# Performance work log

Hardware: AMD Instinct MI355X
Metric: run time of the kernel (lower is better)

The kernel has to match this reference:

```python
import jax, jax.numpy as jnp
import numpy as np

QUERY_DIM = 3072
HEADS = 24
HEAD_DIM = 128
INNER = HEADS * HEAD_DIM  # 3072
MLP_HIDDEN = int(QUERY_DIM * 4.0)  # 12288
MLP_MULT = 2
EPS = 1e-5
B, S = 1, 4096


def setup_inputs() -> dict:
    key = jax.random.key(0)
    ks = jax.random.split(key, 8)
    hidden_states = jax.random.normal(ks[0], (B, S, QUERY_DIM), dtype=jnp.float32)
    # rotary angles for half the head dim (interleaved / non-neox style)
    t = jnp.arange(S, dtype=jnp.float32)[:, None]
    inv_freq = 1.0 / (10000.0 ** (jnp.arange(0, HEAD_DIM, 2, dtype=jnp.float32) / HEAD_DIM))
    ang = t * inv_freq[None, :]
    cos = jnp.cos(ang)
    sin = jnp.sin(ang)
    W_qkv_mlp = jax.random.normal(ks[1], (QUERY_DIM, 3 * INNER + MLP_HIDDEN * MLP_MULT), dtype=jnp.float32) * 0.02
    W_out = jax.random.normal(ks[2], (INNER + MLP_HIDDEN, QUERY_DIM), dtype=jnp.float32) * 0.02
    b_out = jnp.zeros((QUERY_DIM,), dtype=jnp.float32)
    norm_q_w = jnp.ones((HEAD_DIM,), dtype=jnp.float32)
    norm_k_w = jnp.ones((HEAD_DIM,), dtype=jnp.float32)
    return {"hidden_states": hidden_states, "cos": cos, "sin": sin,
            "W_qkv_mlp": W_qkv_mlp, "W_out": W_out, "b_out": b_out,
            "norm_q_w": norm_q_w, "norm_k_w": norm_k_w}


def _rmsnorm(x, w, eps=EPS):
    var = jnp.mean(jnp.square(x), axis=-1, keepdims=True)
    return x * jax.lax.rsqrt(var + eps) * w


def _rope_interleaved(x, cos, sin):
    # x: [B,S,H,D]; cos/sin: [S, D//2]. Non-neox: rotate interleaved pairs.
    x1 = x[..., 0::2]
    x2 = x[..., 1::2]
    c = cos[None, :, None, :]
    s = sin[None, :, None, :]
    o1 = x1 * c - x2 * s
    o2 = x2 * c + x1 * s
    return jnp.stack([o1, o2], axis=-1).reshape(x.shape)


def reference(hidden_states, cos, sin, W_qkv_mlp, W_out, b_out, norm_q_w, norm_k_w):
    h = hidden_states @ W_qkv_mlp  # [B,S, 3*INNER + 2*MLP_HIDDEN]
    qkv, mlp = jnp.split(h, [3 * INNER], axis=-1)
    q, k, v = jnp.split(qkv, 3, axis=-1)
    q = q.reshape(B, S, HEADS, HEAD_DIM)
    k = k.reshape(B, S, HEADS, HEAD_DIM)
    v = v.reshape(B, S, HEADS, HEAD_DIM)
    q = _rmsnorm(q, norm_q_w)
    k = _rmsnorm(k, norm_k_w)
    q = _rope_interleaved(q, cos, sin)
    k = _rope_interleaved(k, cos, sin)
    scale = 1.0 / np.sqrt(HEAD_DIM)
    scores = jnp.einsum('bqhd,bkhd->bhqk', q, k) * scale
    probs = jax.nn.softmax(scores, axis=-1)
    attn = jnp.einsum('bhqk,bkhd->bqhd', probs, v)
    attn = attn.reshape(B, S, INNER)
    m1, m2 = jnp.split(mlp, 2, axis=-1)
    mlp_out = jax.nn.silu(m1) * m2
    out = jnp.concatenate([attn, mlp_out], axis=-1) @ W_out + b_out
    return out
```

## Files before the change

kernel.cpp:

```cpp
#include <hip/hip_runtime.h>

typedef short shortx8 __attribute__((ext_vector_type(8)));
typedef short shortx4 __attribute__((ext_vector_type(4)));
typedef float floatx4 __attribute__((ext_vector_type(4)));
typedef float floatx16 __attribute__((ext_vector_type(16)));
typedef unsigned short u16;
typedef unsigned int u32;

#define GLB(x) ((const __attribute__((address_space(1))) void*)(x))
#define LDSC(x) ((__attribute__((address_space(3))) void*)(x))
#define BARRIER()                                  \
  do {                                             \
    __builtin_amdgcn_sched_barrier(0);             \
    __builtin_amdgcn_s_barrier();                  \
    __builtin_amdgcn_sched_barrier(0);             \
  } while (0)
#define WAITV8() asm volatile("s_waitcnt vmcnt(8)" ::: "memory")

__device__ __forceinline__ float bf2f(u16 u) {
  unsigned x = ((unsigned)u) << 16;
  float f;
  __builtin_memcpy(&f, &x, 4);
  return f;
}
__device__ __forceinline__ u16 f2bf(float f) {
  unsigned x;
  __builtin_memcpy(&x, &f, 4);
  x += 0x7fffu + ((x >> 16) & 1u);
  return (u16)(x >> 16);
}
__device__ __forceinline__ u32 pk_bf16(float lo, float hi) {
  u32 r;
  asm("v_cvt_pk_bf16_f32 %0, %1, %2" : "=v"(r) : "v"(lo), "v"(hi));
  return r;
}

__global__ __launch_bounds__(256) void cast_bf16(const float* __restrict__ src,
                                                 u16* __restrict__ dst) {
  const size_t i = ((size_t)blockIdx.x * 256 + threadIdx.x) << 3;
  floatx4 a = *(const floatx4*)(src + i);
  floatx4 b = *(const floatx4*)(src + i + 4);
  shortx8 o;
#pragma unroll
  for (int e = 0; e < 4; ++e) {
    o[e] = (short)f2bf(a[e]);
    o[e + 4] = (short)f2bf(b[e]);
  }
  *(shortx8*)(dst + i) = o;
}

__global__ __launch_bounds__(256) void transpose_cast(const float* __restrict__ src,
                                                      u16* __restrict__ dst,
                                                      int R, int C, int perm) {
  __shared__ u16 T[64 * 72];
  const int tiles_c = C >> 6;
  const int r0 = (blockIdx.x / tiles_c) << 6;
  const int c0 = (blockIdx.x % tiles_c) << 6;
  const int tid = threadIdx.x;
  const int rl = tid >> 4;
  const int cb = (tid & 15) << 2;
#pragma unroll
  for (int rr = 0; rr < 4; ++rr) {
    const int row = rr * 16 + rl;
    floatx4 v = *(const floatx4*)(src + (size_t)(r0 + row) * C + c0 + cb);
#pragma unroll
    for (int i = 0; i < 4; ++i) T[(cb + i) * 72 + row] = f2bf(v[i]);
  }
  __syncthreads();
  int dbase = c0;
  if (perm && c0 >= 9216) {
    if (c0 < 21504) { const int u = c0 - 9216;  dbase = 9216 + ((u >> 7) << 8) + (u & 64); }
    else            { const int u = c0 - 21504; dbase = 9216 + ((u >> 7) << 8) + 128 + (u & 64); }
  }
#pragma unroll
  for (int ii = 0; ii < 2; ++ii) {
    const int chunk = tid + (ii << 8);
    const int cr = chunk >> 3;
    const int r8 = (chunk & 7) << 3;
    shortx8 v = *(const shortx8*)(T + cr * 72 + r8);
    *(shortx8*)(dst + (size_t)(dbase + cr) * R + r0 + r8) = v;
  }
}

template <int MODE>
__global__ __launch_bounds__(512, 2) void gemm8(const u16* __restrict__ A,
                                                const u16* __restrict__ B,
                                                void* __restrict__ Cout,
                                                u16* __restrict__ CC2,
                                                int M, int N, int K, int Ksub) {
  __shared__ u16 lds[8 * 8192];

  const int nbm = M >> 8;
  const int nwg = nbm * (N >> 8);
  const int cpx = nwg >> 3;
  const int wg = ((int)blockIdx.x & 7) * cpx + ((int)blockIdx.x >> 3);
  const int bm = wg % nbm;
  const int bn = wg / nbm;
  const int koff = (int)blockIdx.y * Ksub;

  const int tid = threadIdx.x;
  const int lane = tid & 63;
  const int w = tid >> 6;
  const int wm = w >> 2;
  const int wn = w & 3;
  const int l15 = lane & 15;
  const int l4 = lane >> 4;
  const int NT = Ksub >> 6;

  const int lrow = lane >> 2;
  const int lblk = lane & 3;

#define UNIT(buf, mat, ks) (lds + (((buf) * 4 + (mat) * 2 + (ks)) << 13))

  const u16* Abase = A + (size_t)bm * 256 * K + koff;
  const u16* Bbase = B + (size_t)bn * 256 * K + koff;

  auto STAGE = [&](int mat, int ks, int buf, int t) {
    const u16* gb = mat ? Bbase : Abase;
#pragma unroll
    for (int j = 0; j < 2; ++j) {
      const int row = (w * 2 + j) * 16 + lrow;
      const int sblk = lblk ^ ((row >> 1) & 3);
      const u16* src = gb + (size_t)row * K + (t << 6) + (ks << 5) + (sblk << 3);
      __builtin_amdgcn_global_load_lds(GLB(src),
                                       LDSC(UNIT(buf, mat, ks) + ((w * 2 + j) << 9)),
                                       16, 0, 0);
    }
  };
  auto LDA = [&](int mf, int ks, int buf) -> shortx8 {
    const int row = wm * 128 + mf * 16 + l15;
    return *(const shortx8*)(UNIT(buf, 0, ks) + row * 32 + ((l4 ^ ((row >> 1) & 3)) << 3));
  };
  auto LDB = [&](int nf, int ks, int buf) -> shortx8 {
    const int row = wn * 64 + nf * 16 + l15;
    return *(const shortx8*)(UNIT(buf, 1, ks) + row * 32 + ((l4 ^ ((row >> 1) & 3)) << 3));
  };

  floatx4 acc[8][4] = {};

  STAGE(0, 0, 0, 0); STAGE(1, 0, 0, 0);
  STAGE(0, 1, 0, 0); STAGE(1, 1, 0, 0);
  STAGE(0, 0, 1, 1); STAGE(1, 0, 1, 1);
  WAITV8();
  BARRIER();

#pragma unroll 2
  for (int T = 0; T < NT; ++T) {
    const int cur = T & 1, nxt = cur ^ 1;
    const int t1 = (T + 1 < NT) ? T + 1 : NT - 1;
    const int t2 = (T + 2 < NT) ? T + 2 : NT - 1;
    shortx8 af[4], bf[4];

#pragma unroll
    for (int m = 0; m < 4; ++m) af[m] = LDA(m, 0, cur);
#pragma unroll
    for (int n = 0; n < 4; ++n) bf[n] = LDB(n, 0, cur);
    STAGE(0, 1, nxt, t1);
    BARRIER();
    __builtin_amdgcn_s_setprio(1);
#pragma unroll
    for (int m = 0; m < 4; ++m)
#pragma unroll
      for (int n = 0; n < 4; ++n)
        acc[m][n] = __builtin_amdgcn_mfma_f32_16x16x32_bf16(af[m], bf[n], acc[m][n], 0, 0, 0);
    __builtin_amdgcn_s_setprio(0);
    BARRIER();

#pragma unroll
    for (int m = 0; m < 4; ++m) af[m] = LDA(4 + m, 0, cur);
    STAGE(1, 1, nxt, t1);
    BARRIER();
    __builtin_amdgcn_s_setprio(1);
#pragma unroll
    for (int m = 0; m < 4; ++m)
#pragma unroll
      for (int n = 0; n < 4; ++n)
        acc[4 + m][n] = __builtin_amdgcn_mfma_f32_16x16x32_bf16(af[m], bf[n], acc[4 + m][n], 0, 0, 0);
    __builtin_amdgcn_s_setprio(0);
    WAITV8();
    BARRIER();

#pragma unroll
    for (int m = 0; m < 4; ++m) af[m] = LDA(m, 1, cur);
#pragma unroll
    for (int n = 0; n < 4; ++n) bf[n] = LDB(n, 1, cur);
    STAGE(0, 0, cur, t2);
    BARRIER();
    __builtin_amdgcn_s_setprio(1);
#pragma unroll
    for (int m = 0; m < 4; ++m)
#pragma unroll
      for (int n = 0; n < 4; ++n)
        acc[m][n] = __builtin_amdgcn_mfma_f32_16x16x32_bf16(af[m], bf[n], acc[m][n], 0, 0, 0);
    __builtin_amdgcn_s_setprio(0);
    BARRIER();

#pragma unroll
    for (int m = 0; m < 4; ++m) af[m] = LDA(4 + m, 1, cur);
    STAGE(1, 0, cur, t2);
    BARRIER();
    __builtin_amdgcn_s_setprio(1);
#pragma unroll
    for (int m = 0; m < 4; ++m)
#pragma unroll
      for (int n = 0; n < 4; ++n)
        acc[4 + m][n] = __builtin_amdgcn_mfma_f32_16x16x32_bf16(af[m], bf[n], acc[4 + m][n], 0, 0, 0);
    __builtin_amdgcn_s_setprio(0);
    WAITV8();
    BARRIER();
  }

  const int orow0 = bm * 256 + wm * 128 + (l4 << 2);
  if (MODE == 0) {
    if (bn < 36) {
      u16* C = (u16*)Cout;
      const int ocol0 = bn * 256 + wn * 64 + l15;
#pragma unroll
      for (int m = 0; m < 8; ++m)
#pragma unroll
        for (int n = 0; n < 4; ++n)
#pragma unroll
          for (int r = 0; r < 4; ++r)
            C[(size_t)(orow0 + m * 16 + r) * 9216 + ocol0 + n * 16] = f2bf(acc[m][n][r]);
    } else {
      __syncthreads();
      float* buf = (float*)lds + (wm * 2 + (wn & 1)) * 8192;
      if (wn >= 2) {
#pragma unroll
        for (int m = 0; m < 4; ++m)
#pragma unroll
          for (int n = 0; n < 4; ++n) {
            const int chunk = (m * 4 + l4) ^ (l15 & 7);
            *(floatx4*)(buf + (((n * 16 + l15) << 4) + chunk) * 4) = acc[m][n];
          }
      } else {
#pragma unroll
        for (int m = 0; m < 4; ++m)
#pragma unroll
          for (int n = 0; n < 4; ++n) {
            const int chunk = (m * 4 + l4) ^ (l15 & 7);
            *(floatx4*)(buf + 4096 + (((n * 16 + l15) << 4) + chunk) * 4) = acc[4 + m][n];
          }
      }
      __syncthreads();
      const int gcol0 = 3072 + (bn - 36) * 128 + (wn & 1) * 64 + l15;
      if (wn < 2) {
#pragma unroll
        for (int m = 0; m < 4; ++m)
#pragma unroll
          for (int n = 0; n < 4; ++n) {
            const int chunk = (m * 4 + l4) ^ (l15 & 7);
            const floatx4 m2v = *(const floatx4*)(buf + (((n * 16 + l15) << 4) + chunk) * 4);
#pragma unroll
            for (int r = 0; r < 4; ++r) {
              const float m1 = acc[m][n][r];
              const float sg = 1.0f / (1.0f + exp2f(-1.4426950408889634f * m1));
              CC2[(size_t)(orow0 + m * 16 + r) * 15360 + gcol0 + n * 16] =
                  f2bf(m1 * sg * m2v[r]);
            }
          }
      } else {
#pragma unroll
        for (int m = 0; m < 4; ++m)
#pragma unroll
          for (int n = 0; n < 4; ++n) {
            const int chunk = (m * 4 + l4) ^ (l15 & 7);
            const floatx4 m1v = *(const floatx4*)(buf + 4096 + (((n * 16 + l15) << 4) + chunk) * 4);
#pragma unroll
            for (int r = 0; r < 4; ++r) {
              const float m1 = m1v[r];
              const float sg = 1.0f / (1.0f + exp2f(-1.4426950408889634f * m1));
              CC2[(size_t)(orow0 + (4 + m) * 16 + r) * 15360 + gcol0 + n * 16] =
                  f2bf(m1 * sg * acc[4 + m][n][r]);
            }
          }
      }
    }
  } else {
    float* C = (float*)Cout + (size_t)blockIdx.y * M * N;
    const int ocol0 = bn * 256 + wn * 64 + l15;
#pragma unroll
    for (int m = 0; m < 8; ++m)
#pragma unroll
      for (int n = 0; n < 4; ++n)
#pragma unroll
        for (int r = 0; r < 4; ++r)
          C[(size_t)(orow0 + m * 16 + r) * N + ocol0 + n * 16] = acc[m][n][r];
  }
}
#undef UNIT

__global__ __launch_bounds__(256) void reduce_bias(const float* __restrict__ P,
                                                   const float* __restrict__ bias,
                                                   float* __restrict__ out) {
  const size_t base = ((size_t)blockIdx.x * 256 + threadIdx.x) << 2;
  const size_t stride = (size_t)4096 * 3072;
  floatx4 a = *(const floatx4*)(P + base);
  floatx4 b = *(const floatx4*)(P + stride + base);
  floatx4 c = *(const floatx4*)(P + 2 * stride + base);
  floatx4 d = *(const floatx4*)(P + 3 * stride + base);
  floatx4 bb = *(const floatx4*)(bias + (base % 3072));
  *(floatx4*)(out + base) = a + b + c + d + bb;
}

#define QSCALE (0.08838834764831845f * 1.4426950408889634f)

__global__ __launch_bounds__(256, 2) void qkv_prep(
    const u16* __restrict__ H, const float* __restrict__ cosb,
    const float* __restrict__ sinb, const float* __restrict__ nqw,
    const float* __restrict__ nkw, u16* __restrict__ Qo, u16* __restrict__ Ko,
    u16* __restrict__ Vo) {
  __shared__ u16 VT[128 * 72];
  const int head = blockIdx.y;
  const int t0 = blockIdx.x << 6;
  const int tid = threadIdx.x;
  const int tl = tid >> 2;
  const int db = (tid & 3) << 5;
  const int token = t0 + tl;

  const u16* hp = H + (size_t)token * 9216 + head * 128 + db;
  shortx8 qv[4], kvv[4], vv[4];
#pragma unroll
  for (int i = 0; i < 4; ++i) {
    qv[i] = *(const shortx8*)(hp + i * 8);
    kvv[i] = *(const shortx8*)(hp + 3072 + i * 8);
    vv[i] = *(const shortx8*)(hp + 6144 + i * 8);
  }
  float qx[32], kx[32];
  float sq = 0.f, sk = 0.f;
#pragma unroll
  for (int i = 0; i < 4; ++i)
#pragma unroll
    for (int j = 0; j < 8; ++j) {
      float a = bf2f((u16)qv[i][j]); qx[i * 8 + j] = a; sq += a * a;
      float b = bf2f((u16)kvv[i][j]); kx[i * 8 + j] = b; sk += b * b;
    }
  sq += __shfl_xor(sq, 1); sq += __shfl_xor(sq, 2);
  sk += __shfl_xor(sk, 1); sk += __shfl_xor(sk, 2);
  const float rq = rsqrtf(sq * (1.0f / 128.0f) + 1e-5f);
  const float rk = rsqrtf(sk * (1.0f / 128.0f) + 1e-5f);

  shortx8 oqv[4], okv[4];
#pragma unroll
  for (int p = 0; p < 16; ++p) {
    const float c = cosb[(size_t)token * 64 + (db >> 1) + p];
    const float s = sinb[(size_t)token * 64 + (db >> 1) + p];
    const int vi = p >> 2, vj = (p & 3) << 1;
    float a1 = qx[2 * p] * rq * nqw[db + 2 * p];
    float a2 = qx[2 * p + 1] * rq * nqw[db + 2 * p + 1];
    oqv[vi][vj] = (short)f2bf((a1 * c - a2 * s) * QSCALE);
    oqv[vi][vj + 1] = (short)f2bf((a2 * c + a1 * s) * QSCALE);
    float b1 = kx[2 * p] * rk * nkw[db + 2 * p];
    float b2 = kx[2 * p + 1] * rk * nkw[db + 2 * p + 1];
    okv[vi][vj] = (short)f2bf(b1 * c - b2 * s);
    okv[vi][vj + 1] = (short)f2bf(b2 * c + b1 * s);
  }
  {
    u16* qo = Qo + (size_t)head * 4096 * 128 + (size_t)token * 128 + db;
    u16* ko = Ko + (size_t)head * 4096 * 128 + (size_t)token * 128 + db;
#pragma unroll
    for (int i = 0; i < 4; ++i) {
      *(shortx8*)(qo + i * 8) = oqv[i];
      *(shortx8*)(ko + i * 8) = okv[i];
    }
  }
#pragma unroll
  for (int i = 0; i < 4; ++i)
#pragma unroll
    for (int j = 0; j < 8; ++j) VT[(db + i * 8 + j) * 72 + tl] = (u16)vv[i][j];
  __syncthreads();
#pragma unroll
  for (int ii = 0; ii < 4; ++ii) {
    const int chunk = tid + (ii << 8);
    const int d = chunk >> 3;
    const int j8 = (chunk & 7) << 3;
    shortx8 v = *(const shortx8*)(VT + d * 72 + j8);
    *(shortx8*)(Vo + (size_t)head * 128 * 4096 + (size_t)d * 4096 + t0 + j8) = v;
  }
}

__global__ __launch_bounds__(256, 2) void attn_kernel(const u16* __restrict__ Qg,
                                                      const u16* __restrict__ Kg,
                                                      const u16* __restrict__ Vg,
                                                      u16* __restrict__ CC) {
  __shared__ u16 Ks[128 * 128];
  __shared__ u16 Vs[128 * 128];

  const int head = blockIdx.y;
  const int q0 = blockIdx.x << 7;
  const int tid = threadIdx.x;
  const int lane = tid & 63;
  const int wave = tid >> 6;
  const int l31 = lane & 31;
  const int kh = lane >> 5;

  const u16* Qh = Qg + (size_t)head * 4096 * 128;
  const u16* Kh = Kg + (size_t)head * 4096 * 128;
  const u16* Vh = Vg + (size_t)head * 128 * 4096;

  const int qrow = q0 + wave * 32 + l31;
  shortx8 qf[8];
#pragma unroll
  for (int ks = 0; ks < 8; ++ks)
    qf[ks] = *(const shortx8*)(Qh + (size_t)qrow * 128 + ks * 16 + kh * 8);

  floatx16 ot[4] = {};
  float mrun = -1e30f, lrun = 0.0f;

  for (int s0 = 0; s0 < 4096; s0 += 128) {
#pragma unroll
    for (int i = 0; i < 8; ++i) {
      const int c = wave * 8 + i;
      const int row = c * 4 + (lane >> 4);
      const int blk = (lane & 15) ^ (row & 7);
      __builtin_amdgcn_global_load_lds(GLB(Kh + (size_t)(s0 + row) * 128 + blk * 8),
                                       LDSC(Ks + c * 512), 16, 0, 0);
    }
#pragma unroll
    for (int i = 0; i < 8; ++i) {
      const int c = wave * 8 + i;
      const int row = c * 4 + (lane >> 4);
      const int blk = (lane & 15) ^ (row & 7);
      __builtin_amdgcn_global_load_lds(GLB(Vh + (size_t)row * 4096 + s0 + blk * 8),
                                       LDSC(Vs + c * 512), 16, 0, 0);
    }
    __syncthreads();

    floatx16 st[4] = {};
    __builtin_amdgcn_s_setprio(1);
#pragma unroll
    for (int kvt = 0; kvt < 4; ++kvt) {
      const int krow = kvt * 32 + l31;
#pragma unroll
      for (int ks = 0; ks < 8; ++ks) {
        shortx8 kf = *(const shortx8*)(Ks + krow * 128 + (((ks * 2 + kh) ^ (krow & 7)) << 3));
        st[kvt] = __builtin_amdgcn_mfma_f32_32x32x16_bf16(kf, qf[ks], st[kvt], 0, 0, 0);
      }
    }
    __builtin_amdgcn_s_setprio(0);

    float vmax = st[0][0];
#pragma unroll
    for (int t = 0; t < 4; ++t)
#pragma unroll
      for (int r = 0; r < 16; ++r) vmax = fmaxf(vmax, st[t][r]);
    vmax = fmaxf(vmax, __shfl_xor(vmax, 32));
    const float mn = fmaxf(mrun, vmax);
    const float alpha = exp2f(mrun - mn);
    mrun = mn;

    float rs = 0.0f;
#pragma unroll
    for (int t = 0; t < 4; ++t)
#pragma unroll
      for (int r = 0; r < 16; ++r) {
        const float p = exp2f(st[t][r] - mn);
        st[t][r] = p;
        rs += p;
      }
    rs += __shfl_xor(rs, 32);
    lrun = lrun * alpha + rs;
    if (__any(alpha < 1.0f)) {
#pragma unroll
      for (int dt = 0; dt < 4; ++dt)
#pragma unroll
        for (int r = 0; r < 16; ++r) ot[dt][r] *= alpha;
    }

    u32 w[4][8];
#pragma unroll
    for (int t = 0; t < 4; ++t)
#pragma unroll
      for (int q = 0; q < 4; ++q) {
        w[t][2 * q] = pk_bf16(st[t][4 * q], st[t][4 * q + 1]);
        w[t][2 * q + 1] = pk_bf16(st[t][4 * q + 2], st[t][4 * q + 3]);
      }

#pragma unroll
    for (int ks = 0; ks < 8; ++ks) {
      const int kvt = ks >> 1;
      const int qA = 2 * (ks & 1);
      const u32 wA0 = w[kvt][2 * qA], wA1 = w[kvt][2 * qA + 1];
      const u32 wB0 = w[kvt][2 * qA + 2], wB1 = w[kvt][2 * qA + 3];
      const u32 send0 = kh ? wA0 : wB0;
      const u32 send1 = kh ? wA1 : wB1;
      const u32 r0 = (u32)__shfl_xor((int)send0, 32);
      const u32 r1 = (u32)__shfl_xor((int)send1, 32);
      u32 fw[4];
      fw[0] = kh ? r0 : wA0;
      fw[1] = kh ? r1 : wA1;
      fw[2] = kh ? wB0 : r0;
      fw[3] = kh ? wB1 : r1;
      shortx8 pf;
      __builtin_memcpy(&pf, fw, 16);
      __builtin_amdgcn_s_setprio(1);
#pragma unroll
      for (int dt = 0; dt < 4; ++dt) {
        const int vrow = dt * 32 + l31;
        shortx8 vf = *(const shortx8*)(Vs + vrow * 128 + (((ks * 2 + kh) ^ (vrow & 7)) << 3));
        ot[dt] = __builtin_amdgcn_mfma_f32_32x32x16_bf16(vf, pf, ot[dt], 0, 0, 0);
      }
      __builtin_amdgcn_s_setprio(0);
    }
    __syncthreads();
  }

  const float inv = 1.0f / lrun;
  u16* outp = CC + (size_t)qrow * 15360 + head * 128;
#pragma unroll
  for (int dt = 0; dt < 4; ++dt)
#pragma unroll
    for (int g = 0; g < 4; ++g) {
      shortx4 pack;
#pragma unroll
      for (int r = 0; r < 4; ++r) pack[r] = (short)f2bf(ot[dt][4 * g + r] * inv);
      *(shortx4*)(outp + dt * 32 + g * 8 + kh * 4) = pack;
    }
}

extern "C" void kernel_launch(void* const* d_in, const int* in_sizes, int n_in,
                              void* d_out, int out_size, void* d_ws, size_t ws_size,
                              hipStream_t stream) {
  const float* hs = (const float*)d_in[0];
  const float* cosb = (const float*)d_in[1];
  const float* sinb = (const float*)d_in[2];
  const float* w1 = (const float*)d_in[3];
  const float* wout = (const float*)d_in[4];
  const float* bout = (const float*)d_in[5];
  const float* nqw = (const float*)d_in[6];
  const float* nkw = (const float*)d_in[7];
  float* out = (float*)d_out;

  char* ws = (char*)d_ws;
  u16* X16 = (u16*)ws; ws += (size_t)4096 * 3072 * 2;
  u16* W1T = (u16*)ws; ws += (size_t)33792 * 3072 * 2;
  u16* WOT = (u16*)ws; ws += (size_t)3072 * 15360 * 2;
  u16* H   = (u16*)ws; ws += (size_t)4096 * 33792 * 2;
  u16* Qb  = (u16*)ws; ws += (size_t)24 * 4096 * 128 * 2;
  u16* Kb  = (u16*)ws; ws += (size_t)24 * 4096 * 128 * 2;
  u16* VTb = (u16*)ws; ws += (size_t)24 * 4096 * 128 * 2;
  u16* CC  = (u16*)ws; ws += (size_t)4096 * 15360 * 2;
  float* Pk = (float*)H;

  cast_bf16<<<6144, 256, 0, stream>>>(hs, X16);
  transpose_cast<<<(3072 / 64) * (33792 / 64), 256, 0, stream>>>(w1, W1T, 3072, 33792, 1);
  transpose_cast<<<(15360 / 64) * (3072 / 64), 256, 0, stream>>>(wout, WOT, 15360, 3072, 0);
  gemm8<0><<<(4096 / 256) * (33792 / 256), 512, 0, stream>>>(X16, W1T, H, CC,
                                                             4096, 33792, 3072, 3072);
  qkv_prep<<<dim3(64, 24), 256, 0, stream>>>(H, cosb, sinb, nqw, nkw, Qb, Kb, VTb);
  attn_kernel<<<dim3(32, 24), 256, 0, stream>>>(Qb, Kb, VTb, CC);
  gemm8<1><<<dim3((4096 / 256) * (3072 / 256), 4), 512, 0, stream>>>(
      CC, WOT, Pk, nullptr, 4096, 3072, 15360, 3840);
  reduce_bias<<<(4096 * 3072 / 4) / 256, 256, 0, stream>>>(Pk, bout, out);
}
```

Before: 1.767 ms.

## Software-pipeline LDS fragment loads against MFMA in GEMM main loop

Restructures the GEMM inner loop so the A/B fragment reads from LDS for the next MFMA block are issued before the current MFMA block runs. Fine-grained lgkmcnt waits replace some of the barriers. Global-to-LDS staging waits change from vmcnt(8) to vmcnt(6), and the loop now has four barriers per iteration instead of eight. This aims to hide LDS latency and cut barrier stalls, at the cost of more live registers and a tighter buffer-reuse ordering that could race.

```diff
diff --git a/kernel.cpp b/kernel.cpp
--- a/kernel.cpp
+++ b/kernel.cpp
@@ -15,7 +15,13 @@
     __builtin_amdgcn_s_barrier();                  \
     __builtin_amdgcn_sched_barrier(0);             \
   } while (0)
+#define WAITV6() asm volatile("s_waitcnt vmcnt(6)" ::: "memory")
 #define WAITV8() asm volatile("s_waitcnt vmcnt(8)" ::: "memory")
+#define WAITLGKM(N)                                          \
+  do {                                                       \
+    asm volatile("s_waitcnt lgkmcnt(" #N ")");               \
+    __builtin_amdgcn_sched_barrier(0);                       \
+  } while (0)
 
 __device__ __forceinline__ float bf2f(u16 u) {
   unsigned x = ((unsigned)u) << 16;
@@ -137,76 +143,80 @@
   };
 
   floatx4 acc[8][4] = {};
+  shortx8 a_cur[4], a_nxt[4], b_cur[4], b_nxt[4];
 
   STAGE(0, 0, 0, 0); STAGE(1, 0, 0, 0);
   STAGE(0, 1, 0, 0); STAGE(1, 1, 0, 0);
   STAGE(0, 0, 1, 1); STAGE(1, 0, 1, 1);
   WAITV8();
   BARRIER();
+#pragma unroll
+  for (int m = 0; m < 4; ++m) a_cur[m] = LDA(m, 0, 0);
+#pragma unroll
+  for (int n = 0; n < 4; ++n) b_cur[n] = LDB(n, 0, 0);
 
 #pragma unroll 2
   for (int T = 0; T < NT; ++T) {
     const int cur = T & 1, nxt = cur ^ 1;
     const int t1 = (T + 1 < NT) ? T + 1 : NT - 1;
     const int t2 = (T + 2 < NT) ? T + 2 : NT - 1;
-    shortx8 af[4], bf[4];
-
-#pragma unroll
-    for (int m = 0; m < 4; ++m) af[m] = LDA(m, 0, cur);
-#pragma unroll
-    for (int n = 0; n < 4; ++n) bf[n] = LDB(n, 0, cur);
+
     STAGE(0, 1, nxt, t1);
+#pragma unroll
+    for (int m = 0; m < 4; ++m) a_nxt[m] = LDA(4 + m, 0, cur);
+    WAITLGKM(4);
+    __builtin_amdgcn_s_setprio(1);
+#pragma unroll
+    for (int m = 0; m < 4; ++m)
+#pragma unroll
+      for (int n = 0; n < 4; ++n)
+        acc[m][n] = __builtin_amdgcn_mfma_f32_16x16x32_bf16(a_cur[m], b_cur[n], acc[m][n], 0, 0, 0);
+    __builtin_amdgcn_s_setprio(0);
+    WAITV6();
     BARRIER();
+
+    STAGE(1, 1, nxt, t1);
+#pragma unroll
+    for (int m = 0; m < 4; ++m) a_cur[m] = LDA(m, 1, cur);
+#pragma unroll
+    for (int n = 0; n < 4; ++n) b_nxt[n] = LDB(n, 1, cur);
+    WAITLGKM(8);
     __builtin_amdgcn_s_setprio(1);
 #pragma unroll
     for (int m = 0; m < 4; ++m)
 #pragma unroll
       for (int n = 0; n < 4; ++n)
-        acc[m][n] = __builtin_amdgcn_mfma_f32_16x16x32_bf16(af[m], bf[n], acc[m][n], 0, 0, 0);
+        acc[4 + m][n] = __builtin_amdgcn_mfma_f32_16x16x32_bf16(a_nxt[m], b_cur[n], acc[4 + m][n], 0, 0, 0);
     __builtin_amdgcn_s_setprio(0);
     BARRIER();
 
-#pragma unroll
-    for (int m = 0; m < 4; ++m) af[m] = LDA(4 + m, 0, cur);
-    STAGE(1, 1, nxt, t1);
+    STAGE(0, 0, cur, t2);
+#pragma unroll
+    for (int m = 0; m < 4; ++m) a_nxt[m] = LDA(4 + m, 1, cur);
+    WAITLGKM(4);
+    __builtin_amdgcn_s_setprio(1);
+#pragma unroll
+    for (int m = 0; m < 4; ++m)
+#pragma unroll
+      for (int n = 0; n < 4; ++n)
+        acc[m][n] = __builtin_amdgcn_mfma_f32_16x16x32_bf16(a_cur[m], b_nxt[n], acc[m][n], 0, 0, 0);
+    __builtin_amdgcn_s_setprio(0);
+    WAITV6();
     BARRIER();
+
+    STAGE(1, 0, cur, t2);
+#pragma unroll
+    for (int m = 0; m < 4; ++m) a_cur[m] = LDA(m, 0, nxt);
+#pragma unroll
+    for (int n = 0; n < 4; ++n) b_cur[n] = LDB(n, 0, nxt);
+    WAITLGKM(8);
     __builtin_amdgcn_s_setprio(1);
 #pragma unroll
     for (int m = 0; m < 4; ++m)
 #pragma unroll
       for (int n = 0; n < 4; ++n)
-        acc[4 + m][n] = __builtin_amdgcn_mfma_f32_16x16x32_bf16(af[m], bf[n], acc[4 + m][n], 0, 0, 0);
+        acc[4 + m][n] = __builtin_amdgcn_mfma_f32_16x16x32_bf16(a_nxt[m], b_nxt[n], acc[4 + m][n], 0, 0, 0);
     __builtin_amdgcn_s_setprio(0);
-    WAITV8();
-    BARRIER();
-
-#pragma unroll
-    for (int m = 0; m < 4; ++m) af[m] = LDA(m, 1, cur);
-#pragma unroll
-    for (int n = 0; n < 4; ++n) bf[n] = LDB(n, 1, cur);
-    STAGE(0, 0, cur, t2);
-    BARRIER();
-    __builtin_amdgcn_s_setprio(1);
-#pragma unroll
-    for (int m = 0; m < 4; ++m)
-#pragma unroll
-      for (int n = 0; n < 4; ++n)
-        acc[m][n] = __builtin_amdgcn_mfma_f32_16x16x32_bf16(af[m], bf[n], acc[m][n], 0, 0, 0);
-    __builtin_amdgcn_s_setprio(0);
-    BARRIER();
-
-#pragma unroll
-    for (int m = 0; m < 4; ++m) af[m] = LDA(4 + m, 1, cur);
-    STAGE(1, 0, cur, t2);
-    BARRIER();
-    __builtin_amdgcn_s_setprio(1);
-#pragma unroll
-    for (int m = 0; m < 4; ++m)
-#pragma unroll
-      for (int n = 0; n < 4; ++n)
-        acc[4 + m][n] = __builtin_amdgcn_mfma_f32_16x16x32_bf16(af[m], bf[n], acc[4 + m][n], 0, 0, 0);
-    __builtin_amdgcn_s_setprio(0);
-    WAITV8();
     BARRIER();
   }
 
```

New measurement: 1.746 ms. About the same (-1.2%).
